# Kernel tuning notes

Measured on AMD Instinct MI355X. Metric: run time of the kernel, lower is better.

Reference implementation:

```python
import jax, jax.numpy as jnp
import numpy as np
from jax import lax

T, B = 80, 32
ACT, CIN, HID, LSTM_H = 16, 4, 512, 256

def _conv(x, w, b, stride, pad):
    y = lax.conv_general_dilated(x, w, (stride, stride), [(pad, pad), (pad, pad)],
                                 dimension_numbers=('NCHW', 'OIHW', 'NCHW'))
    return y + b[None, :, None, None]

def setup_inputs() -> dict:
    key = jax.random.key(0)
    ks = jax.random.split(key, 20)
    s = 0.02
    return {
        'x': jax.random.uniform(ks[0], (T, B, CIN, 84, 84), dtype=jnp.float32),
        'last_action': jax.random.randint(ks[1], (T, B), 0, ACT),
        'reward': jax.random.normal(ks[2], (T, B), dtype=jnp.float32),
        'dones': jnp.zeros((T, B), dtype=bool),
        'hx': jax.random.normal(ks[3], (2, B, LSTM_H), dtype=jnp.float32) * s,
        'conv1_w': jax.random.normal(ks[4], (32, CIN, 8, 8), jnp.float32) * s,
        'conv1_b': jnp.zeros((32,), jnp.float32),
        'conv2_w': jax.random.normal(ks[5], (64, 32, 4, 4), jnp.float32) * s,
        'conv2_b': jnp.zeros((64,), jnp.float32),
        'conv3_w': jax.random.normal(ks[6], (64, 64, 3, 3), jnp.float32) * s,
        'conv3_b': jnp.zeros((64,), jnp.float32),
        'fc_w': jax.random.normal(ks[7], (HID, 3136), jnp.float32) * s,
        'fc_b': jnp.zeros((HID,), jnp.float32),
        'lstm_wih': jax.random.normal(ks[8], (4 * LSTM_H, HID + ACT + 1), jnp.float32) * s,
        'lstm_whh': jax.random.normal(ks[9], (4 * LSTM_H, LSTM_H), jnp.float32) * s,
        'lstm_bih': jnp.zeros((4 * LSTM_H,), jnp.float32),
        'lstm_bhh': jnp.zeros((4 * LSTM_H,), jnp.float32),
        'actor_w': jax.random.normal(ks[10], (ACT, LSTM_H), jnp.float32) * s,
        'actor_b': jnp.zeros((ACT,), jnp.float32),
        'critic_w': jax.random.normal(ks[11], (1, LSTM_H), jnp.float32) * s,
        'critic_b': jnp.zeros((1,), jnp.float32),
    }

def reference(x, last_action, reward, dones, hx,
              conv1_w, conv1_b, conv2_w, conv2_b, conv3_w, conv3_b,
              fc_w, fc_b, lstm_wih, lstm_whh, lstm_bih, lstm_bhh,
              actor_w, actor_b, critic_w, critic_b):
    seq_len, bs = x.shape[0], x.shape[1]
    xf = x.reshape(seq_len * bs, CIN, 84, 84)          # combine time & batch
    la = jax.nn.one_hot(last_action.reshape(-1), ACT, dtype=jnp.float32)
    rw = reward.reshape(-1, 1)

    lrelu = lambda v: jax.nn.leaky_relu(v, 0.01)
    h = lrelu(_conv(xf, conv1_w, conv1_b, 4, 1))       # [N,32,20,20]
    h = lrelu(_conv(h, conv2_w, conv2_b, 2, 0))        # [N,64,9,9]
    h = lrelu(_conv(h, conv3_w, conv3_b, 1, 0))        # [N,64,7,7]
    h = h.reshape(h.shape[0], -1)                      # [N,3136]
    h = lrelu(h @ fc_w.T + fc_b)                       # [N,512]
    h = jnp.concatenate([h, rw, la], axis=1)           # [N,529]
    h = h.reshape(seq_len, bs, -1)

    def step(carry, inp):
        xt, dt = inp                                   # [bs,529], [bs] bool
        carry = jnp.where(dt[None, :, None], 0.0, carry)
        hh, cc = carry[0], carry[1]
        gates = xt @ lstm_wih.T + lstm_bih + hh @ lstm_whh.T + lstm_bhh
        i, f, g, o = jnp.split(gates, 4, axis=1)
        cc = jax.nn.sigmoid(f) * cc + jax.nn.sigmoid(i) * jnp.tanh(g)
        hh = jax.nn.sigmoid(o) * jnp.tanh(cc)
        return jnp.stack([hh, cc], 0), hh

    _, hs = lax.scan(step, hx, (h, dones))             # hs: [T,bs,256]
    feat = hs.reshape(seq_len * bs, LSTM_H)

    logits = feat @ actor_w.T + actor_b                # [N,16]
    values = feat @ critic_w.T + critic_b              # [N,1]
    logits = jnp.where(jnp.isnan(logits), jnp.float32(1e-12), logits)
    return logits.reshape(seq_len, -1, bs), values.reshape(seq_len, bs)
```

## Files before the change

### kernel.cpp

```cpp
#include <hip/hip_runtime.h>
#include <math.h>

#define T_ 80
#define B_ 32
#define N_ 2560
#define LH_ 256

typedef __attribute__((ext_vector_type(8))) short short8;
typedef __attribute__((ext_vector_type(4))) float f32x4;
#define MFMA16(a, b, c) __builtin_amdgcn_mfma_f32_16x16x32_bf16((a), (b), (c), 0, 0, 0)

__device__ __forceinline__ float lrelu(float v) { return v > 0.f ? v : 0.01f * v; }
__device__ __forceinline__ short f2bf(float f) {
    unsigned u = __float_as_uint(f);
    return (short)((u + 0x7fffu + ((u >> 16) & 1u)) >> 16);
}

__global__ void pack1_k(const float* __restrict__ w, short* __restrict__ d) {
    int g = blockIdx.x * 256 + threadIdx.x;
    int ky = g >> 10, oc = (g >> 5) & 31, k = g & 31, kx = k >> 2, ci = k & 3;
    d[g] = f2bf(w[((oc * 4 + ci) * 8 + ky) * 8 + kx]);
}
__global__ void pack2_k(const float* __restrict__ w, short* __restrict__ d) {
    int g = blockIdx.x * 256 + threadIdx.x;
    int t = g >> 11, oc = (g >> 5) & 63, ci = g & 31, ky = t >> 2, kx = t & 3;
    d[g] = f2bf(w[((oc * 32 + ci) * 4 + ky) * 4 + kx]);
}
__global__ void pack3_k(const float* __restrict__ w, short* __restrict__ d) {
    int g = blockIdx.x * 256 + threadIdx.x;
    int tkc = g >> 11, oc = (g >> 5) & 63, c32 = g & 31;
    int t = tkc >> 1, kc = tkc & 1, ky = t / 3, kx = t % 3;
    d[g] = f2bf(w[((oc * 64 + kc * 32 + c32) * 3 + ky) * 3 + kx]);
}
__global__ void packfc_k(const float* __restrict__ w, short* __restrict__ d) {
    int g = blockIdx.x * 256 + threadIdx.x;
    int j = g / 3136, kp = g % 3136, p = kp >> 6, oc = kp & 63;
    d[g] = f2bf(w[j * 3136 + oc * 49 + p]);
}
__global__ void packih_k(const float* __restrict__ w, short* __restrict__ d) {
    int g = blockIdx.x * 256 + threadIdx.x;
    int r = g >> 9, k = g & 511;
    d[g] = f2bf(w[r * 529 + k]);
}
__global__ void zero_flags_k(int* __restrict__ flags) { flags[threadIdx.x] = 0; }

#define C1_RS 344
__global__ __launch_bounds__(512) void conv1_mfma(
    const float* __restrict__ x, const short* __restrict__ wp1,
    const float* __restrict__ bias, short* __restrict__ h1) {
    __shared__ short xs[44 * C1_RS];
    __shared__ short ob[208 * 32];
    int blk = blockIdx.x, n = blk >> 1, h = blk & 1, tid = threadIdx.x;
    for (int i = tid; i < 44 * 84; i += 512) {
        int ry = i / 84, xi4 = i % 84;
        int ci = xi4 / 21, x4 = xi4 % 21;
        int iy = ry + h * 40 - 1;
        if (iy < 0 || iy > 83) continue;
        float4 v = *(const float4*)(x + (size_t)(n * 4 + ci) * 7056 + iy * 84 + x4 * 4);
        int base = ry * C1_RS + (x4 * 4 + 1) * 4 + ci;
        xs[base] = f2bf(v.x); xs[base + 4] = f2bf(v.y);
        xs[base + 8] = f2bf(v.z); xs[base + 12] = f2bf(v.w);
    }
    for (int i = tid; i < 44 * 4; i += 512)
        xs[(i >> 2) * C1_RS + (i & 3)] = 0;
    if (h == 0) for (int i = tid; i < C1_RS; i += 512) xs[i] = 0;
    __syncthreads();

    int lane = tid & 63, wid = tid >> 6;
    int lr = lane & 15, kq = lane >> 4;
    short8 bfr[8][2];
#pragma unroll
    for (int ky = 0; ky < 8; ++ky)
#pragma unroll
        for (int nt = 0; nt < 2; ++nt)
            bfr[ky][nt] = *(const short8*)&wp1[((ky * 32) + nt * 16 + lr) * 32 + kq * 8];
    float b0 = bias[lr], b1 = bias[16 + lr];

    for (int t = wid; t < 13; t += 8) {
        int p = t * 16 + lr; if (p > 199) p = 199;
        int oy = p / 20, ox = p % 20;
        f32x4 acc0 = {0.f, 0.f, 0.f, 0.f}, acc1 = {0.f, 0.f, 0.f, 0.f};
#pragma unroll
        for (int ky = 0; ky < 8; ++ky) {
            int ry = oy * 4 + ky;
            short8 af = *(const short8*)&xs[ry * C1_RS + ox * 16 + kq * 8];
            acc0 = MFMA16(af, bfr[ky][0], acc0);
            acc1 = MFMA16(af, bfr[ky][1], acc1);
        }
        int pm = t * 16 + kq * 4;
#pragma unroll
        for (int r = 0; r < 4; ++r) {
            ob[(pm + r) * 32 + lr]      = f2bf(lrelu(acc0[r] + b0));
            ob[(pm + r) * 32 + 16 + lr] = f2bf(lrelu(acc1[r] + b1));
        }
    }
    __syncthreads();
    uint4* dst = (uint4*)(h1 + (size_t)n * 12800 + h * 6400);
    for (int i = tid; i < 800; i += 512) dst[i] = ((uint4*)ob)[i];
}

__global__ __launch_bounds__(512) void conv2_mfma(
    const short* __restrict__ h1, const short* __restrict__ wp2,
    const float* __restrict__ bias, short* __restrict__ h2) {
    __shared__ short in_s[400 * 40];
    __shared__ short ob[96 * 64];
    int n = blockIdx.x, tid = threadIdx.x;
    const uint4* src = (const uint4*)(h1 + (size_t)n * 12800);
    for (int i = tid; i < 1600; i += 512) {
        *(uint4*)&in_s[(i >> 2) * 40 + (i & 3) * 8] = src[i];
    }
    __syncthreads();
    int lane = tid & 63, wid = tid >> 6;
    int nt = wid & 3, mh = wid >> 2;
    int lr = lane & 15, kq = lane >> 4;
    short8 bfr[16];
#pragma unroll
    for (int t = 0; t < 16; ++t)
        bfr[t] = *(const short8*)&wp2[(t * 64 + nt * 16 + lr) * 32 + kq * 8];
    float bl = bias[nt * 16 + lr];
    for (int mt = mh * 3; mt < mh * 3 + 3; ++mt) {
        int p = mt * 16 + lr; if (p > 80) p = 80;
        int oy = p / 9, ox = p % 9;
        f32x4 acc = {0.f, 0.f, 0.f, 0.f};
#pragma unroll
        for (int ky = 0; ky < 4; ++ky)
#pragma unroll
            for (int kx = 0; kx < 4; ++kx) {
                int pix = (oy * 2 + ky) * 20 + ox * 2 + kx;
                short8 af = *(const short8*)&in_s[pix * 40 + kq * 8];
                acc = MFMA16(af, bfr[ky * 4 + kx], acc);
            }
        int pm = mt * 16 + kq * 4;
#pragma unroll
        for (int r = 0; r < 4; ++r)
            ob[(pm + r) * 64 + nt * 16 + lr] = f2bf(lrelu(acc[r] + bl));
    }
    __syncthreads();
    uint4* dst = (uint4*)(h2 + (size_t)n * 5184);
    for (int i = tid; i < 648; i += 512) dst[i] = ((uint4*)ob)[i];
}

__global__ __launch_bounds__(512) void conv3_mfma(
    const short* __restrict__ h2, const short* __restrict__ wp3,
    const float* __restrict__ bias, short* __restrict__ h3) {
    __shared__ short in_s[81 * 72];
    __shared__ short ob[64 * 64];
    int n = blockIdx.x, tid = threadIdx.x;
    const uint4* src = (const uint4*)(h2 + (size_t)n * 5184);
    for (int i = tid; i < 648; i += 512) {
        *(uint4*)&in_s[(i >> 3) * 72 + (i & 7) * 8] = src[i];
    }
    __syncthreads();
    int lane = tid & 63, wid = tid >> 6;
    int nt = wid & 3, mh = wid >> 2;
    int lr = lane & 15, kq = lane >> 4;
    short8 bfr[18];
#pragma unroll
    for (int t = 0; t < 18; ++t)
        bfr[t] = *(const short8*)&wp3[(t * 64 + nt * 16 + lr) * 32 + kq * 8];
    float bl = bias[nt * 16 + lr];
    for (int mt = mh * 2; mt < mh * 2 + 2; ++mt) {
        int p = mt * 16 + lr; if (p > 48) p = 48;
        int oy = p / 7, ox = p % 7;
        f32x4 acc = {0.f, 0.f, 0.f, 0.f};
#pragma unroll
        for (int ky = 0; ky < 3; ++ky)
#pragma unroll
            for (int kx = 0; kx < 3; ++kx) {
                int pix = (oy + ky) * 9 + ox + kx;
#pragma unroll
                for (int kc = 0; kc < 2; ++kc) {
                    short8 af = *(const short8*)&in_s[pix * 72 + kc * 32 + kq * 8];
                    acc = MFMA16(af, bfr[(ky * 3 + kx) * 2 + kc], acc);
                }
            }
        int pm = mt * 16 + kq * 4;
#pragma unroll
        for (int r = 0; r < 4; ++r)
            ob[(pm + r) * 64 + nt * 16 + lr] = f2bf(lrelu(acc[r] + bl));
    }
    __syncthreads();
    uint4* dst = (uint4*)(h3 + (size_t)n * 3136);
    for (int i = tid; i < 392; i += 512) dst[i] = ((uint4*)ob)[i];
}

template <int OUT>
__global__ __launch_bounds__(256) void gemm_bf16(
    const short* __restrict__ A, const short* __restrict__ B,
    const float* __restrict__ bias, void* __restrict__ Cout,
    int M, int N, int K, int ldc) {
    __shared__ short smem[20480];
    int m0 = blockIdx.y * 128, n0 = blockIdx.x * 128;
    int tid = threadIdx.x;
    int lane = tid & 63, wid = tid >> 6;
    int wr = wid >> 1, wc = wid & 1;
    int lr = lane & 15, kq = lane >> 4;
    f32x4 acc[4][4];
#pragma unroll
    for (int i = 0; i < 4; ++i)
#pragma unroll
        for (int j = 0; j < 4; ++j) acc[i][j] = (f32x4){0.f, 0.f, 0.f, 0.f};

    int nsteps = K >> 5;
#define STAGE(k0, buf)                                                          \
    {                                                                           \
        short* As = smem + (buf) * 5120;                                        \
        short* Bs = smem + 10240 + (buf) * 5120;                                \
        for (int i = tid; i < 512; i += 256) {                                  \
            int row = i >> 2, c4 = i & 3;                                       \
            *(uint4*)&As[row * 40 + c4 * 8] =                                   \
                *(const uint4*)&A[(size_t)(m0 + row) * K + (k0) + c4 * 8];      \
            *(uint4*)&Bs[row * 40 + c4 * 8] =                                   \
                *(const uint4*)&B[(size_t)(n0 + row) * K + (k0) + c4 * 8];      \
        }                                                                       \
    }
    STAGE(0, 0);
    __syncthreads();
    for (int ks = 0; ks < nsteps; ++ks) {
        int buf = ks & 1;
        if (ks + 1 < nsteps) STAGE((ks + 1) * 32, buf ^ 1);
        short* As = smem + buf * 5120;
        short* Bs = smem + 10240 + buf * 5120;
        short8 af[4], bfr[4];
#pragma unroll
        for (int i = 0; i < 4; ++i)
            af[i] = *(const short8*)&As[(wr * 64 + i * 16 + lr) * 40 + kq * 8];
#pragma unroll
        for (int j = 0; j < 4; ++j)
            bfr[j] = *(const short8*)&Bs[(wc * 64 + j * 16 + lr) * 40 + kq * 8];
#pragma unroll
        for (int i = 0; i < 4; ++i)
#pragma unroll
            for (int j = 0; j < 4; ++j)
                acc[i][j] = MFMA16(af[i], bfr[j], acc[i][j]);
        __syncthreads();
    }
#undef STAGE
    if (OUT == 0) {
        float* C = (float*)Cout;
#pragma unroll
        for (int i = 0; i < 4; ++i)
#pragma unroll
            for (int j = 0; j < 4; ++j)
#pragma unroll
                for (int r = 0; r < 4; ++r) {
                    int row = m0 + wr * 64 + i * 16 + kq * 4 + r;
                    int col = n0 + wc * 64 + j * 16 + lr;
                    C[(size_t)row * ldc + col] = acc[i][j][r];
                }
    } else {
        short* ob = smem;
#pragma unroll
        for (int i = 0; i < 4; ++i)
#pragma unroll
            for (int j = 0; j < 4; ++j) {
                int col = wc * 64 + j * 16 + lr;
                float bl = bias[n0 + col];
#pragma unroll
                for (int r = 0; r < 4; ++r) {
                    int row = wr * 64 + i * 16 + kq * 4 + r;
                    ob[row * 128 + col] = f2bf(lrelu(acc[i][j][r] + bl));
                }
            }
        __syncthreads();
        short* C = (short*)Cout;
        for (int i = tid; i < 2048; i += 256) {
            int row = i >> 4, c16 = i & 15;
            *(uint4*)&C[(size_t)(m0 + row) * ldc + n0 + c16 * 8] =
                *(uint4*)&ob[row * 128 + c16 * 8];
        }
    }
}

__global__ void gx_epi_k(float* __restrict__ gx, const float* __restrict__ reward,
                         const int* __restrict__ la, const float* __restrict__ wih,
                         const float* __restrict__ bih, const float* __restrict__ bhh) {
    int gid = blockIdx.x * 256 + threadIdx.x;
    int n = gid >> 10, j = gid & 1023;
    const float* wr = wih + (size_t)j * 529;
    gx[gid] += bih[j] + bhh[j] + reward[n] * wr[512] + wr[513 + la[n]];
}

__global__ __launch_bounds__(512) void lstm16_k(
    const float* __restrict__ gx,
    const float* __restrict__ whh,
    const unsigned char* __restrict__ dones,
    const float* __restrict__ hx,
    float* __restrict__ hs,
    float* __restrict__ hpub,
    int* __restrict__ cnt) {
    const int tid = threadIdx.x;
    const int grp  = blockIdx.x & 7;
    const int half = blockIdx.x >> 3;
    const int lane = tid & 63, w = tid >> 6;
    const int gt = w >> 1, s2 = w & 1;
    const int lr = lane & 15, kq = lane >> 4;

    __shared__ short hB[16 * 264];
    __shared__ float gate_s[4][128][4];

    short8 afr[4][8];
#pragma unroll
    for (int mi = 0; mi < 4; ++mi) {
        int row = gt * 256 + half * 128 + s2 * 64 + mi * 16 + lr;
        const float* wr = whh + (size_t)row * 256;
#pragma unroll
        for (int kt = 0; kt < 8; ++kt) {
            int k0 = kt * 32 + kq * 8;
            float4 a = *(const float4*)(wr + k0);
            float4 b = *(const float4*)(wr + k0 + 4);
            short8 f;
            f[0] = f2bf(a.x); f[1] = f2bf(a.y); f[2] = f2bf(a.z); f[3] = f2bf(a.w);
            f[4] = f2bf(b.x); f[5] = f2bf(b.y); f[6] = f2bf(b.z); f[7] = f2bf(b.w);
            afr[mi][kt] = f;
        }
    }
    {
        int* ap = (int*)afr;
#pragma unroll
        for (int i = 0; i < 128; ++i) asm volatile("" : "+v"(ap[i]));
    }

    for (int i = tid; i < 12 * 264; i += 512) hB[4 * 264 + i] = 0;

    const int u = tid >> 2, bt = tid & 3;
    const int b = grp * 4 + bt, gu = half * 128 + u;
    float cc = hx[(size_t)B_ * LH_ + b * LH_ + gu];
    __syncthreads();

    const int mycnt = (grp * 2 + half) * 32, peercnt = (grp * 2 + (half ^ 1)) * 32;

    for (int t = 1; t <= T_; ++t) {
        const int nb0 = (t - 1) * B_;
        float gxv[4];
#pragma unroll
        for (int g2 = 0; g2 < 4; ++g2)
            gxv[g2] = gx[(size_t)(nb0 + b) * 1024 + g2 * 256 + gu];

        if (t > 1) {
            if (tid == 0) {
                while (__hip_atomic_load(&cnt[peercnt], __ATOMIC_ACQUIRE,
                                         __HIP_MEMORY_SCOPE_AGENT) < t - 1)
                    __builtin_amdgcn_s_sleep(1);
            }
            __syncthreads();
        }
#pragma unroll
        for (int l = 0; l < 2; ++l) {
            int e = tid + l * 512;
            int bt2 = e >> 8, k = e & 255;
            int b2 = grp * 4 + bt2;
            float hv = (t == 1) ? hx[b2 * LH_ + k]
                                : hpub[((t - 1) & 1) * 8192 + b2 * 256 + k];
            if (dones[nb0 + b2]) hv = 0.f;
            hB[bt2 * 264 + k] = f2bf(hv);
        }
        __syncthreads();

        f32x4 acc[4] = {{0.f,0.f,0.f,0.f},{0.f,0.f,0.f,0.f},
                        {0.f,0.f,0.f,0.f},{0.f,0.f,0.f,0.f}};
#pragma unroll
        for (int kt = 0; kt < 8; ++kt) {
            short8 bfr = *(const short8*)&hB[lr * 264 + kt * 32 + kq * 8];
#pragma unroll
            for (int mi = 0; mi < 4; ++mi)
                acc[mi] = MFMA16(afr[mi][kt], bfr, acc[mi]);
        }
        if (lr < 4) {
#pragma unroll
            for (int mi = 0; mi < 4; ++mi)
#pragma unroll
                for (int r = 0; r < 4; ++r)
                    gate_s[gt][s2 * 64 + mi * 16 + kq * 4 + r][lr] = acc[mi][r];
        }
        __syncthreads();

        {
            bool dn = dones[nb0 + b] != 0;
            float gi = gate_s[0][u][bt] + gxv[0];
            float gf = gate_s[1][u][bt] + gxv[1];
            float gg = gate_s[2][u][bt] + gxv[2];
            float go = gate_s[3][u][bt] + gxv[3];
            float ccv = dn ? 0.f : cc;
            float si = 1.f / (1.f + expf(-gi));
            float sf = 1.f / (1.f + expf(-gf));
            float so = 1.f / (1.f + expf(-go));
            float c2 = sf * ccv + si * tanhf(gg);
            float h2 = so * tanhf(c2);
            cc = c2;
            hs[(size_t)(nb0 + b) * LH_ + gu] = h2;
            __hip_atomic_store(&hpub[(t & 1) * 8192 + b * 256 + gu], h2,
                               __ATOMIC_RELAXED, __HIP_MEMORY_SCOPE_AGENT);
        }
        __syncthreads();
        if (tid == 0)
            __hip_atomic_store(&cnt[mycnt], t, __ATOMIC_RELEASE,
                               __HIP_MEMORY_SCOPE_AGENT);
    }
}

__global__ void head_k(const float* __restrict__ hs,
                       const float* __restrict__ aw, const float* __restrict__ ab,
                       const float* __restrict__ cw, const float* __restrict__ cb,
                       float* __restrict__ out) {
    int gid = blockIdx.x * 256 + threadIdx.x;
    if (gid >= N_ * 17) return;
    int n = gid / 17, r = gid % 17;
    const float* f = hs + (size_t)n * 256;
    if (r < 16) {
        const float* w = aw + r * 256;
        float acc = ab[r];
        for (int k = 0; k < 256; ++k) acc = fmaf(f[k], w[k], acc);
        if (isnan(acc)) acc = 1e-12f;
        out[(size_t)n * 16 + r] = acc;
    } else {
        float acc = cb[0];
        for (int k = 0; k < 256; ++k) acc = fmaf(f[k], cw[k], acc);
        out[(size_t)N_ * 16 + n] = acc;
    }
}

extern "C" void kernel_launch(void* const* d_in, const int* in_sizes, int n_in,
                              void* d_out, int out_size, void* d_ws, size_t ws_size,
                              hipStream_t stream) {
    const float* x      = (const float*)d_in[0];
    const int* la       = (const int*)d_in[1];
    const float* reward = (const float*)d_in[2];
    const unsigned char* dones = (const unsigned char*)d_in[3];
    const float* hx     = (const float*)d_in[4];
    const float* c1w = (const float*)d_in[5];  const float* c1b = (const float*)d_in[6];
    const float* c2w = (const float*)d_in[7];  const float* c2b = (const float*)d_in[8];
    const float* c3w = (const float*)d_in[9];  const float* c3b = (const float*)d_in[10];
    const float* fcw = (const float*)d_in[11]; const float* fcb = (const float*)d_in[12];
    const float* wih = (const float*)d_in[13]; const float* whh = (const float*)d_in[14];
    const float* bih = (const float*)d_in[15]; const float* bhh = (const float*)d_in[16];
    const float* aw  = (const float*)d_in[17]; const float* ab  = (const float*)d_in[18];
    const float* cw  = (const float*)d_in[19]; const float* cb  = (const float*)d_in[20];

    char* wsb = (char*)d_ws;
    short* h1   = (short*)(wsb);
    short* h2   = (short*)(wsb + 65536000);
    short* h3   = (short*)(wsb + 92078080);
    short* hfc  = (short*)(wsb + 108134400);
    float* gx   = (float*)(wsb + 110755840);
    float* hs   = (float*)(wsb + 121241600);
    float* hpub = (float*)(wsb + 123863040);
    int*   cnt  = (int*)  (wsb + 123928576);
    short* wp1  = (short*)(wsb + 123932672);
    short* wp2  = (short*)(wsb + 123949056);
    short* wp3  = (short*)(wsb + 124014592);
    short* wfcP = (short*)(wsb + 124088320);
    short* wihP = (short*)(wsb + 127299584);

    pack1_k<<<32, 256, 0, stream>>>(c1w, wp1);
    pack2_k<<<128, 256, 0, stream>>>(c2w, wp2);
    pack3_k<<<144, 256, 0, stream>>>(c3w, wp3);
    packfc_k<<<6272, 256, 0, stream>>>(fcw, wfcP);
    packih_k<<<2048, 256, 0, stream>>>(wih, wihP);
    zero_flags_k<<<1, 512, 0, stream>>>(cnt);

    conv1_mfma<<<5120, 512, 0, stream>>>(x, wp1, c1b, h1);
    conv2_mfma<<<2560, 512, 0, stream>>>(h1, wp2, c2b, h2);
    conv3_mfma<<<2560, 512, 0, stream>>>(h2, wp3, c3b, h3);

    gemm_bf16<1><<<dim3(4, 20), 256, 0, stream>>>(h3, wfcP, fcb, hfc, 2560, 512, 3136, 512);
    gemm_bf16<0><<<dim3(8, 20), 256, 0, stream>>>(hfc, wihP, nullptr, gx, 2560, 1024, 512, 1024);
    gx_epi_k<<<10240, 256, 0, stream>>>(gx, reward, la, wih, bih, bhh);

    lstm16_k<<<16, 512, 0, stream>>>(gx, whh, dones, hx, hs, hpub, cnt);
    head_k<<<170, 256, 0, stream>>>(hs, aw, ab, cw, cb, (float*)d_out);
}
```

Measured before the change: 570.1 us.

## Fuse conv2/conv3, pack kernels, gx epilogue, and streamline LSTM handoff

Merges the five weight-pack kernels and the flag zeroing into one launch. Fuses conv2 and conv3 into a single kernel that keeps the conv2 output in shared memory, so the h2 intermediate never goes to global memory. Folds the bias, reward and one-hot action terms into the second GEMM's epilogue and drops the separate gx_epi kernel. In the LSTM, every thread now spins on the peer flag instead of one thread plus a barrier, reads only the peer half of h from hpub, and writes its own half into shared memory directly. The dones masking moves to the producer step, which is a more delicate ordering to get right.

```diff
diff --git a/kernel.cpp b/kernel.cpp
--- a/kernel.cpp
+++ b/kernel.cpp
@@ -16,33 +16,50 @@
     return (short)((u + 0x7fffu + ((u >> 16) & 1u)) >> 16);
 }
 
-__global__ void pack1_k(const float* __restrict__ w, short* __restrict__ d) {
-    int g = blockIdx.x * 256 + threadIdx.x;
-    int ky = g >> 10, oc = (g >> 5) & 31, k = g & 31, kx = k >> 2, ci = k & 3;
-    d[g] = f2bf(w[((oc * 4 + ci) * 8 + ky) * 8 + kx]);
-}
-__global__ void pack2_k(const float* __restrict__ w, short* __restrict__ d) {
-    int g = blockIdx.x * 256 + threadIdx.x;
-    int t = g >> 11, oc = (g >> 5) & 63, ci = g & 31, ky = t >> 2, kx = t & 3;
-    d[g] = f2bf(w[((oc * 32 + ci) * 4 + ky) * 4 + kx]);
-}
-__global__ void pack3_k(const float* __restrict__ w, short* __restrict__ d) {
-    int g = blockIdx.x * 256 + threadIdx.x;
-    int tkc = g >> 11, oc = (g >> 5) & 63, c32 = g & 31;
-    int t = tkc >> 1, kc = tkc & 1, ky = t / 3, kx = t % 3;
-    d[g] = f2bf(w[((oc * 64 + kc * 32 + c32) * 3 + ky) * 3 + kx]);
-}
-__global__ void packfc_k(const float* __restrict__ w, short* __restrict__ d) {
-    int g = blockIdx.x * 256 + threadIdx.x;
-    int j = g / 3136, kp = g % 3136, p = kp >> 6, oc = kp & 63;
-    d[g] = f2bf(w[j * 3136 + oc * 49 + p]);
-}
-__global__ void packih_k(const float* __restrict__ w, short* __restrict__ d) {
-    int g = blockIdx.x * 256 + threadIdx.x;
-    int r = g >> 9, k = g & 511;
-    d[g] = f2bf(w[r * 529 + k]);
-}
-__global__ void zero_flags_k(int* __restrict__ flags) { flags[threadIdx.x] = 0; }
+__global__ void pack_all_k(const float* __restrict__ c1w, const float* __restrict__ c2w,
+                           const float* __restrict__ c3w, const float* __restrict__ fcw,
+                           const float* __restrict__ wih,
+                           short* __restrict__ wp1, short* __restrict__ wp2,
+                           short* __restrict__ wp3, short* __restrict__ wfcP,
+                           short* __restrict__ wihP, int* __restrict__ cnt) {
+    int blk = blockIdx.x, tidx = threadIdx.x;
+    if (blk < 6272) {
+        int g = blk * 256 + tidx;
+        int j = g / 3136, kp = g % 3136, p = kp >> 6, oc = kp & 63;
+        wfcP[g] = f2bf(fcw[j * 3136 + oc * 49 + p]);
+        return;
+    }
+    blk -= 6272;
+    if (blk < 2048) {
+        int g = blk * 256 + tidx;
+        int r = g >> 9, k = g & 511;
+        wihP[g] = f2bf(wih[r * 529 + k]);
+        return;
+    }
+    blk -= 2048;
+    if (blk < 32) {
+        int g = blk * 256 + tidx;
+        int ky = g >> 10, oc = (g >> 5) & 31, k = g & 31, kx = k >> 2, ci = k & 3;
+        wp1[g] = f2bf(c1w[((oc * 4 + ci) * 8 + ky) * 8 + kx]);
+        return;
+    }
+    blk -= 32;
+    if (blk < 128) {
+        int g = blk * 256 + tidx;
+        int t = g >> 11, oc = (g >> 5) & 63, ci = g & 31, ky = t >> 2, kx = t & 3;
+        wp2[g] = f2bf(c2w[((oc * 32 + ci) * 4 + ky) * 4 + kx]);
+        return;
+    }
+    blk -= 128;
+    if (blk < 144) {
+        int g = blk * 256 + tidx;
+        int tkc = g >> 11, oc = (g >> 5) & 63, c32 = g & 31;
+        int t = tkc >> 1, kc = tkc & 1, ky = t / 3, kx = t % 3;
+        wp3[g] = f2bf(c3w[((oc * 64 + kc * 32 + c32) * 3 + ky) * 3 + kx]);
+        return;
+    }
+    cnt[tidx] = 0; cnt[256 + tidx] = 0;
+}
 
 #define C1_RS 344
 __global__ __launch_bounds__(512) void conv1_mfma(
@@ -99,96 +116,87 @@
     for (int i = tid; i < 800; i += 512) dst[i] = ((uint4*)ob)[i];
 }
 
-__global__ __launch_bounds__(512) void conv2_mfma(
-    const short* __restrict__ h1, const short* __restrict__ wp2,
-    const float* __restrict__ bias, short* __restrict__ h2) {
+__global__ __launch_bounds__(512) void conv23_mfma(
+    const short* __restrict__ h1,
+    const short* __restrict__ wp2, const float* __restrict__ b2v,
+    const short* __restrict__ wp3, const float* __restrict__ b3v,
+    short* __restrict__ h3) {
     __shared__ short in_s[400 * 40];
-    __shared__ short ob[96 * 64];
+    __shared__ short ob2[96 * 72];
     int n = blockIdx.x, tid = threadIdx.x;
     const uint4* src = (const uint4*)(h1 + (size_t)n * 12800);
-    for (int i = tid; i < 1600; i += 512) {
+    for (int i = tid; i < 1600; i += 512)
         *(uint4*)&in_s[(i >> 2) * 40 + (i & 3) * 8] = src[i];
-    }
     __syncthreads();
     int lane = tid & 63, wid = tid >> 6;
     int nt = wid & 3, mh = wid >> 2;
     int lr = lane & 15, kq = lane >> 4;
-    short8 bfr[16];
-#pragma unroll
-    for (int t = 0; t < 16; ++t)
-        bfr[t] = *(const short8*)&wp2[(t * 64 + nt * 16 + lr) * 32 + kq * 8];
-    float bl = bias[nt * 16 + lr];
-    for (int mt = mh * 3; mt < mh * 3 + 3; ++mt) {
-        int p = mt * 16 + lr; if (p > 80) p = 80;
-        int oy = p / 9, ox = p % 9;
-        f32x4 acc = {0.f, 0.f, 0.f, 0.f};
-#pragma unroll
-        for (int ky = 0; ky < 4; ++ky)
-#pragma unroll
-            for (int kx = 0; kx < 4; ++kx) {
-                int pix = (oy * 2 + ky) * 20 + ox * 2 + kx;
-                short8 af = *(const short8*)&in_s[pix * 40 + kq * 8];
-                acc = MFMA16(af, bfr[ky * 4 + kx], acc);
-            }
-        int pm = mt * 16 + kq * 4;
-#pragma unroll
-        for (int r = 0; r < 4; ++r)
-            ob[(pm + r) * 64 + nt * 16 + lr] = f2bf(lrelu(acc[r] + bl));
-    }
-    __syncthreads();
-    uint4* dst = (uint4*)(h2 + (size_t)n * 5184);
-    for (int i = tid; i < 648; i += 512) dst[i] = ((uint4*)ob)[i];
-}
-
-__global__ __launch_bounds__(512) void conv3_mfma(
-    const short* __restrict__ h2, const short* __restrict__ wp3,
-    const float* __restrict__ bias, short* __restrict__ h3) {
-    __shared__ short in_s[81 * 72];
-    __shared__ short ob[64 * 64];
-    int n = blockIdx.x, tid = threadIdx.x;
-    const uint4* src = (const uint4*)(h2 + (size_t)n * 5184);
-    for (int i = tid; i < 648; i += 512) {
-        *(uint4*)&in_s[(i >> 3) * 72 + (i & 7) * 8] = src[i];
-    }
-    __syncthreads();
-    int lane = tid & 63, wid = tid >> 6;
-    int nt = wid & 3, mh = wid >> 2;
-    int lr = lane & 15, kq = lane >> 4;
-    short8 bfr[18];
-#pragma unroll
-    for (int t = 0; t < 18; ++t)
-        bfr[t] = *(const short8*)&wp3[(t * 64 + nt * 16 + lr) * 32 + kq * 8];
-    float bl = bias[nt * 16 + lr];
-    for (int mt = mh * 2; mt < mh * 2 + 2; ++mt) {
-        int p = mt * 16 + lr; if (p > 48) p = 48;
-        int oy = p / 7, ox = p % 7;
-        f32x4 acc = {0.f, 0.f, 0.f, 0.f};
-#pragma unroll
-        for (int ky = 0; ky < 3; ++ky)
-#pragma unroll
-            for (int kx = 0; kx < 3; ++kx) {
-                int pix = (oy + ky) * 9 + ox + kx;
-#pragma unroll
-                for (int kc = 0; kc < 2; ++kc) {
-                    short8 af = *(const short8*)&in_s[pix * 72 + kc * 32 + kq * 8];
-                    acc = MFMA16(af, bfr[(ky * 3 + kx) * 2 + kc], acc);
+    {
+        short8 bfr[16];
+#pragma unroll
+        for (int t = 0; t < 16; ++t)
+            bfr[t] = *(const short8*)&wp2[(t * 64 + nt * 16 + lr) * 32 + kq * 8];
+        float bl = b2v[nt * 16 + lr];
+        for (int mt = mh * 3; mt < mh * 3 + 3; ++mt) {
+            int p = mt * 16 + lr; if (p > 80) p = 80;
+            int oy = p / 9, ox = p % 9;
+            f32x4 acc = {0.f, 0.f, 0.f, 0.f};
+#pragma unroll
+            for (int ky = 0; ky < 4; ++ky)
+#pragma unroll
+                for (int kx = 0; kx < 4; ++kx) {
+                    int pix = (oy * 2 + ky) * 20 + ox * 2 + kx;
+                    short8 af = *(const short8*)&in_s[pix * 40 + kq * 8];
+                    acc = MFMA16(af, bfr[ky * 4 + kx], acc);
                 }
-            }
-        int pm = mt * 16 + kq * 4;
-#pragma unroll
-        for (int r = 0; r < 4; ++r)
-            ob[(pm + r) * 64 + nt * 16 + lr] = f2bf(lrelu(acc[r] + bl));
+            int pm = mt * 16 + kq * 4;
+#pragma unroll
+            for (int r = 0; r < 4; ++r)
+                ob2[(pm + r) * 72 + nt * 16 + lr] = f2bf(lrelu(acc[r] + bl));
+        }
+    }
+    __syncthreads();
+    {
+        short8 cfr[18];
+#pragma unroll
+        for (int t = 0; t < 18; ++t)
+            cfr[t] = *(const short8*)&wp3[(t * 64 + nt * 16 + lr) * 32 + kq * 8];
+        float bl3 = b3v[nt * 16 + lr];
+        short* ob3 = in_s;
+        for (int mt = mh * 2; mt < mh * 2 + 2; ++mt) {
+            int p = mt * 16 + lr; if (p > 48) p = 48;
+            int oy = p / 7, ox = p % 7;
+            f32x4 acc = {0.f, 0.f, 0.f, 0.f};
+#pragma unroll
+            for (int ky = 0; ky < 3; ++ky)
+#pragma unroll
+                for (int kx = 0; kx < 3; ++kx) {
+                    int pix = (oy + ky) * 9 + ox + kx;
+#pragma unroll
+                    for (int kc = 0; kc < 2; ++kc) {
+                        short8 af = *(const short8*)&ob2[pix * 72 + kc * 32 + kq * 8];
+                        acc = MFMA16(af, cfr[(ky * 3 + kx) * 2 + kc], acc);
+                    }
+                }
+            int pm = mt * 16 + kq * 4;
+#pragma unroll
+            for (int r = 0; r < 4; ++r)
+                ob3[(pm + r) * 64 + nt * 16 + lr] = f2bf(lrelu(acc[r] + bl3));
+        }
     }
     __syncthreads();
     uint4* dst = (uint4*)(h3 + (size_t)n * 3136);
-    for (int i = tid; i < 392; i += 512) dst[i] = ((uint4*)ob)[i];
+    for (int i = tid; i < 392; i += 512) dst[i] = ((uint4*)in_s)[i];
 }
 
 template <int OUT>
 __global__ __launch_bounds__(256) void gemm_bf16(
     const short* __restrict__ A, const short* __restrict__ B,
     const float* __restrict__ bias, void* __restrict__ Cout,
-    int M, int N, int K, int ldc) {
+    int M, int N, int K, int ldc,
+    const float* __restrict__ reward = nullptr, const int* __restrict__ la = nullptr,
+    const float* __restrict__ wih = nullptr, const float* __restrict__ bih = nullptr,
+    const float* __restrict__ bhh = nullptr) {
     __shared__ short smem[20480];
     int m0 = blockIdx.y * 128, n0 = blockIdx.x * 128;
     int tid = threadIdx.x;
@@ -236,18 +244,23 @@
         __syncthreads();
     }
 #undef STAGE
-    if (OUT == 0) {
+    if (OUT == 2) {
         float* C = (float*)Cout;
 #pragma unroll
         for (int i = 0; i < 4; ++i)
 #pragma unroll
-            for (int j = 0; j < 4; ++j)
+            for (int j = 0; j < 4; ++j) {
+                int col = n0 + wc * 64 + j * 16 + lr;
+                const float* wrow = wih + (size_t)col * 529;
+                float base = bih[col] + bhh[col];
+                float w512 = wrow[512];
 #pragma unroll
                 for (int r = 0; r < 4; ++r) {
                     int row = m0 + wr * 64 + i * 16 + kq * 4 + r;
-                    int col = n0 + wc * 64 + j * 16 + lr;
-                    C[(size_t)row * ldc + col] = acc[i][j][r];
+                    C[(size_t)row * ldc + col] =
+                        acc[i][j][r] + base + reward[row] * w512 + wrow[513 + la[row]];
                 }
+            }
     } else {
         short* ob = smem;
 #pragma unroll
@@ -270,15 +283,6 @@
                 *(uint4*)&ob[row * 128 + c16 * 8];
         }
     }
-}
-
-__global__ void gx_epi_k(float* __restrict__ gx, const float* __restrict__ reward,
-                         const int* __restrict__ la, const float* __restrict__ wih,
-                         const float* __restrict__ bih, const float* __restrict__ bhh) {
-    int gid = blockIdx.x * 256 + threadIdx.x;
-    int n = gid >> 10, j = gid & 1023;
-    const float* wr = wih + (size_t)j * 529;
-    gx[gid] += bih[j] + bhh[j] + reward[n] * wr[512] + wr[513 + la[n]];
 }
 
 __global__ __launch_bounds__(512) void lstm16_k(
@@ -303,12 +307,12 @@
 #pragma unroll
     for (int mi = 0; mi < 4; ++mi) {
         int row = gt * 256 + half * 128 + s2 * 64 + mi * 16 + lr;
-        const float* wr = whh + (size_t)row * 256;
+        const float* wrp = whh + (size_t)row * 256;
 #pragma unroll
         for (int kt = 0; kt < 8; ++kt) {
             int k0 = kt * 32 + kq * 8;
-            float4 a = *(const float4*)(wr + k0);
-            float4 b = *(const float4*)(wr + k0 + 4);
+            float4 a = *(const float4*)(wrp + k0);
+            float4 b = *(const float4*)(wrp + k0 + 4);
             short8 f;
             f[0] = f2bf(a.x); f[1] = f2bf(a.y); f[2] = f2bf(a.z); f[3] = f2bf(a.w);
             f[4] = f2bf(b.x); f[5] = f2bf(b.y); f[6] = f2bf(b.z); f[7] = f2bf(b.w);
@@ -326,6 +330,16 @@
     const int u = tid >> 2, bt = tid & 3;
     const int b = grp * 4 + bt, gu = half * 128 + u;
     float cc = hx[(size_t)B_ * LH_ + b * LH_ + gu];
+
+#pragma unroll
+    for (int l = 0; l < 2; ++l) {
+        int e = tid + l * 512;
+        int bt2 = e >> 8, k = e & 255;
+        int b2 = grp * 4 + bt2;
+        float hv = hx[b2 * LH_ + k];
+        if (dones[b2]) hv = 0.f;
+        hB[bt2 * 264 + k] = f2bf(hv);
+    }
     __syncthreads();
 
     const int mycnt = (grp * 2 + half) * 32, peercnt = (grp * 2 + (half ^ 1)) * 32;
@@ -338,22 +352,15 @@
             gxv[g2] = gx[(size_t)(nb0 + b) * 1024 + g2 * 256 + gu];
 
         if (t > 1) {
-            if (tid == 0) {
-                while (__hip_atomic_load(&cnt[peercnt], __ATOMIC_ACQUIRE,
-                                         __HIP_MEMORY_SCOPE_AGENT) < t - 1)
-                    __builtin_amdgcn_s_sleep(1);
-            }
-            __syncthreads();
-        }
-#pragma unroll
-        for (int l = 0; l < 2; ++l) {
-            int e = tid + l * 512;
-            int bt2 = e >> 8, k = e & 255;
-            int b2 = grp * 4 + bt2;
-            float hv = (t == 1) ? hx[b2 * LH_ + k]
-                                : hpub[((t - 1) & 1) * 8192 + b2 * 256 + k];
-            if (dones[nb0 + b2]) hv = 0.f;
-            hB[bt2 * 264 + k] = f2bf(hv);
+            while (__hip_atomic_load(&cnt[peercnt], __ATOMIC_RELAXED,
+                                     __HIP_MEMORY_SCOPE_AGENT) < t - 1)
+                __builtin_amdgcn_s_sleep(1);
+            __builtin_amdgcn_fence(__ATOMIC_ACQUIRE, "agent");
+            int pu = tid & 127, bt2 = tid >> 7;
+            int b2 = grp * 4 + bt2, pgu = ((half ^ 1) << 7) + pu;
+            float hv = __hip_atomic_load(&hpub[((t - 1) & 1) * 8192 + b2 * 256 + pgu],
+                                         __ATOMIC_RELAXED, __HIP_MEMORY_SCOPE_AGENT);
+            hB[bt2 * 264 + pgu] = f2bf(hv);
         }
         __syncthreads();
 
@@ -389,8 +396,12 @@
             float h2 = so * tanhf(c2);
             cc = c2;
             hs[(size_t)(nb0 + b) * LH_ + gu] = h2;
-            __hip_atomic_store(&hpub[(t & 1) * 8192 + b * 256 + gu], h2,
-                               __ATOMIC_RELAXED, __HIP_MEMORY_SCOPE_AGENT);
+            if (t < T_) {
+                float hm = dones[t * B_ + b] ? 0.f : h2;
+                hB[bt * 264 + gu] = f2bf(hm);
+                __hip_atomic_store(&hpub[(t & 1) * 8192 + b * 256 + gu], hm,
+                                   __ATOMIC_RELAXED, __HIP_MEMORY_SCOPE_AGENT);
+            }
         }
         __syncthreads();
         if (tid == 0)
@@ -439,7 +450,6 @@
 
     char* wsb = (char*)d_ws;
     short* h1   = (short*)(wsb);
-    short* h2   = (short*)(wsb + 65536000);
     short* h3   = (short*)(wsb + 92078080);
     short* hfc  = (short*)(wsb + 108134400);
     float* gx   = (float*)(wsb + 110755840);
@@ -452,20 +462,17 @@
     short* wfcP = (short*)(wsb + 124088320);
     short* wihP = (short*)(wsb + 127299584);
 
-    pack1_k<<<32, 256, 0, stream>>>(c1w, wp1);
-    pack2_k<<<128, 256, 0, stream>>>(c2w, wp2);
-    pack3_k<<<144, 256, 0, stream>>>(c3w, wp3);
-    packfc_k<<<6272, 256, 0, stream>>>(fcw, wfcP);
-    packih_k<<<2048, 256, 0, stream>>>(wih, wihP);
-    zero_flags_k<<<1, 512, 0, stream>>>(cnt);
+    pack_all_k<<<8625, 256, 0, stream>>>(c1w, c2w, c3w, fcw, wih,
+                                         wp1, wp2, wp3, wfcP, wihP, cnt);
 
     conv1_mfma<<<5120, 512, 0, stream>>>(x, wp1, c1b, h1);
-    conv2_mfma<<<2560, 512, 0, stream>>>(h1, wp2, c2b, h2);
-    conv3_mfma<<<2560, 512, 0, stream>>>(h2, wp3, c3b, h3);
-
-    gemm_bf16<1><<<dim3(4, 20), 256, 0, stream>>>(h3, wfcP, fcb, hfc, 2560, 512, 3136, 512);
-    gemm_bf16<0><<<dim3(8, 20), 256, 0, stream>>>(hfc, wihP, nullptr, gx, 2560, 1024, 512, 1024);
-    gx_epi_k<<<10240, 256, 0, stream>>>(gx, reward, la, wih, bih, bhh);
+    conv23_mfma<<<2560, 512, 0, stream>>>(h1, wp2, c2b, wp3, c3b, h3);
+
+    gemm_bf16<1><<<dim3(4, 20), 256, 0, stream>>>(h3, wfcP, fcb, hfc,
+                                                  2560, 512, 3136, 512);
+    gemm_bf16<2><<<dim3(8, 20), 256, 0, stream>>>(hfc, wihP, nullptr, gx,
+                                                  2560, 1024, 512, 1024,
+                                                  reward, la, wih, bih, bhh);
 
     lstm16_k<<<16, 512, 0, stream>>>(gx, whh, dones, hx, hs, hpub, cnt);
     head_k<<<170, 256, 0, stream>>>(hs, aw, ab, cw, cb, (float*)d_out);
```

After: 622.8 us. +9.2%, slower.
